# Performance work log

Hardware: AMD Instinct MI355X
Metric: run time of the kernel (lower is better)

Reference implementation:

```python
import jax, jax.numpy as jnp
import numpy as np

EPS = 1e-5
TEMP = 0.07
LARGE_NEG = -1e9


def mi_net(x, W1, g1, b1, W2, b2, Ws, lng, lnb):
    # x: (B, C, T). 1x1 convs == per-position channel projections.
    y = jnp.einsum('bct,oc->bot', x, W1)                      # conv1 (no bias)
    mu = y.mean(axis=(0, 2), keepdims=True)                   # BatchNorm2d, training-mode batch stats
    var = y.var(axis=(0, 2), keepdims=True)
    y = (y - mu) * jax.lax.rsqrt(var + EPS) * g1[None, :, None] + b1[None, :, None]
    y = jax.nn.relu(y)
    y = jnp.einsum('bot,po->bpt', y, W2) + b2[None, :, None]  # conv2 (bias)
    h = y + jnp.einsum('bct,oc->bot', x, Ws)                  # linear shortcut
    mu2 = h.mean(axis=1, keepdims=True)                       # LayerNorm over channel dim
    v2 = h.var(axis=1, keepdims=True)
    return (h - mu2) * jax.lax.rsqrt(v2 + EPS) * lng[None, :, None] + lnb[None, :, None]


def infonce(L, G):
    # L: (N, D, T) locals, G: (N, D) single global per sample (n_multis = 1)
    N, D, T = L.shape
    l_p = jnp.swapaxes(L, 1, 2)                               # (N, T, D)
    l_p = l_p / jnp.linalg.norm(l_p, axis=2, keepdims=True)
    g = G / jnp.linalg.norm(G, axis=1, keepdims=True)         # (N, D)
    u_p = (jnp.einsum('ntd,nd->nt', l_p, g) / TEMP)[:, :, None]   # (N, T, 1), positives scaled by temp
    # negatives: <global_i, local_{j,t}>; NOT divided by temperature (faithful to torch source)
    u_n = jnp.einsum('nd,mtd->nmt', g, l_p)                   # (N, N, T)
    eye = jnp.eye(N, dtype=bool)[:, :, None]
    u_n = jnp.where(eye, LARGE_NEG, u_n).reshape(N, N * T)    # mask self pairs
    logits = jnp.concatenate(
        [u_p, jnp.broadcast_to(u_n[:, None, :], (N, T, N * T))], axis=2)  # (N, T, 1+N*T)
    logp = jax.nn.log_softmax(logits, axis=2)
    return -logp[:, :, 0].mean()


def setup_inputs() -> dict:
    key = jax.random.key(0)
    ks = jax.random.split(key, 10)
    B, CL, CG, T, MI = 32, 1536, 192, 256, 512
    d = {
        'local_feat': jax.random.normal(ks[0], (B, CL, T), jnp.float32),
        'global_feat': jax.random.normal(ks[1], (B, CG), jnp.float32),
        # local_net params
        'lW1': jax.random.normal(ks[2], (MI, CL), jnp.float32) * 0.02,
        'lg1': jnp.ones((MI,), jnp.float32),
        'lb1': jnp.zeros((MI,), jnp.float32),
        'lW2': jax.random.normal(ks[3], (MI, MI), jnp.float32) * 0.02,
        'lb2': jnp.zeros((MI,), jnp.float32),
        'lWs': jax.random.normal(ks[4], (MI, CL), jnp.float32) * 0.02,
        'llng': jnp.ones((MI,), jnp.float32),
        'llnb': jnp.zeros((MI,), jnp.float32),
        # global_net params (global_channels != mi_units -> net exists)
        'gW1': jax.random.normal(ks[5], (MI, CG), jnp.float32) * 0.02,
        'gg1': jnp.ones((MI,), jnp.float32),
        'gb1': jnp.zeros((MI,), jnp.float32),
        'gW2': jax.random.normal(ks[6], (MI, MI), jnp.float32) * 0.02,
        'gb2': jnp.zeros((MI,), jnp.float32),
    }
    # shortcut with near-identity init (n_units >= n_input for global net)
    gWs = jax.random.uniform(ks[7], (MI, CG), jnp.float32, -0.01, 0.01)
    gWs = gWs.at[jnp.arange(CG), jnp.arange(CG)].set(1.0)
    d['gWs'] = gWs
    d['glng'] = jnp.ones((MI,), jnp.float32)
    d['glnb'] = jnp.zeros((MI,), jnp.float32)
    return d


def reference(local_feat, global_feat,
              lW1, lg1, lb1, lW2, lb2, lWs, llng, llnb,
              gW1, gg1, gb1, gW2, gb2, gWs, glng, glnb):
    L = mi_net(local_feat, lW1, lg1, lb1, lW2, lb2, lWs, llng, llnb)      # (B, MI, T)
    G = mi_net(global_feat[:, :, None], gW1, gg1, gb1, gW2, gb2, gWs, glng, glnb)[:, :, 0]  # (B, MI)
    return infonce(L, G)
```

## Files before the change

kernel.cpp:

```cpp
#include <hip/hip_runtime.h>

#define B 32
#define CL 1536
#define CG 192
#define T 256
#define MI 512
#define NPOS 8192
#define EPS 1e-5f
#define TEMP 0.07f

typedef __attribute__((ext_vector_type(8))) __bf16 bf16x8;
typedef __attribute__((ext_vector_type(4))) float f32x4;

__device__ __forceinline__ unsigned short f2bf(float f) {
  union { float f; unsigned u; } v; v.f = f;
  unsigned r = v.u + 0x7FFFu + ((v.u >> 16) & 1u);
  return (unsigned short)(r >> 16);
}
__device__ __forceinline__ float bf2f(unsigned short h) {
  union { unsigned u; float f; } v; v.u = ((unsigned)h) << 16;
  return v.f;
}

__device__ __forceinline__ float wave_sum(float v) {
#pragma unroll
  for (int off = 32; off > 0; off >>= 1) v += __shfl_xor(v, off, 64);
  return v;
}
__device__ __forceinline__ float block_sum(float v, float* rb) {
  v = wave_sum(v);
  __syncthreads();
  if ((threadIdx.x & 63) == 0) rb[threadIdx.x >> 6] = v;
  __syncthreads();
  return rb[0] + rb[1] + rb[2] + rb[3];
}
__device__ __forceinline__ float bs128(float v, float* rb) {
  v = wave_sum(v);
  __syncthreads();
  if ((threadIdx.x & 63) == 0) rb[threadIdx.x >> 6] = v;
  __syncthreads();
  return rb[0] + rb[1];
}

__global__ __launch_bounds__(256) void k_prep(
    const float* __restrict__ x, const float* __restrict__ lW1,
    const float* __restrict__ lWs, const float* __restrict__ lW2,
    const float* __restrict__ gx, const float* __restrict__ gW1,
    unsigned short* __restrict__ xT, unsigned short* __restrict__ Wc,
    unsigned short* __restrict__ W2b, float* __restrict__ y1g,
    float* __restrict__ bsum) {
  __shared__ float xs[64][65];
  const int bi = blockIdx.x, tid = threadIdx.x;
  if (bi < 1792) {
    int idx = (bi * 256 + tid) * 4;
    const float* src; unsigned short* dst;
    if (idx < 786432) { src = lW1 + idx; dst = Wc + idx; }
    else if (idx < 1572864) { src = lWs + (idx - 786432); dst = Wc + idx; }
    else { src = lW2 + (idx - 1572864); dst = W2b + (idx - 1572864); }
    float4 v = *(const float4*)src;
    ushort4 o = {f2bf(v.x), f2bf(v.y), f2bf(v.z), f2bf(v.w)};
    *(ushort4*)dst = o;
  } else if (bi < 4864) {
    int bi2 = bi - 1792;
    int b = bi2 / 96, rem = bi2 - b * 96;
    int c0 = (rem >> 2) * 64, t0 = (rem & 3) * 64;
    const float* xb = x + ((size_t)b * CL + c0) * T + t0;
#pragma unroll
    for (int i = 0; i < 16; i++) {
      int idx = tid + i * 256, c = idx >> 6, t = idx & 63;
      xs[c][t] = xb[(size_t)c * T + t];
    }
    __syncthreads();
    unsigned short* ob = xT + ((size_t)b * T + t0) * CL + c0;
#pragma unroll
    for (int half = 0; half < 2; half++) {
      int s = tid + half * 256;
      int t = s >> 3, kg = s & 7;
      unsigned short v[8];
#pragma unroll
      for (int j = 0; j < 8; j++) v[j] = f2bf(xs[kg * 8 + j][t]);
      uint4 o = {(unsigned)v[0] | ((unsigned)v[1] << 16),
                 (unsigned)v[2] | ((unsigned)v[3] << 16),
                 (unsigned)v[4] | ((unsigned)v[5] << 16),
                 (unsigned)v[6] | ((unsigned)v[7] << 16)};
      *(uint4*)&ob[(size_t)t * CL + kg * 8] = o;
    }
  } else if (bi < 4928) {
    int idx = (bi - 4864) * 256 + tid;
    int b = idx & 31, o = idx >> 5;
    float s = 0.f;
    for (int c = 0; c < CG; c++) s = fmaf(gx[b * CG + c], gW1[o * CG + c], s);
    y1g[o * 32 + b] = s;
  } else {
    float4 z = {0.f, 0.f, 0.f, 0.f};
    ((float4*)bsum)[tid] = z;
  }
}

__global__ __launch_bounds__(128, 2) void k_gemm1(
    const unsigned short* __restrict__ xT, const unsigned short* __restrict__ Wc,
    unsigned short* __restrict__ y1u, unsigned short* __restrict__ ysb,
    float* __restrict__ bsum, float* __restrict__ bsq,
    const float* __restrict__ y1g, const float* __restrict__ gg1,
    const float* __restrict__ gb1, const float* __restrict__ gW2,
    const float* __restrict__ gb2, const float* __restrict__ gx,
    const float* __restrict__ gWsc, float* __restrict__ hg) {
  const int tid = threadIdx.x, bi = blockIdx.x;
  if (bi >= 1024) {
    __shared__ float gsc[512], gsh[512];
#pragma unroll
    for (int jj = 0; jj < 4; jj++) {
      int o = tid + jj * 128;
      float s = 0.f, s2 = 0.f;
      for (int b = 0; b < 32; b++) {
        float v = y1g[o * 32 + b];
        s += v; s2 = fmaf(v, v, s2);
      }
      float mu = s * (1.f / 32.f);
      float var = s2 * (1.f / 32.f) - mu * mu;
      float sc = gg1[o] * rsqrtf(var + EPS);
      gsc[o] = sc;
      gsh[o] = gb1[o] - mu * sc;
    }
    __syncthreads();
    int base = (bi - 1024) * 256;
#pragma unroll
    for (int jj = 0; jj < 2; jj++) {
      int idx = base + jj * 128 + tid;
      int b = idx & 31, p = idx >> 5;
      float s = gb2[p];
      for (int o = 0; o < MI; o++) {
        float v = fmaxf(fmaf(y1g[o * 32 + b], gsc[o], gsh[o]), 0.f);
        s = fmaf(v, gW2[(size_t)p * MI + o], s);
      }
      for (int c = 0; c < CG; c++) s = fmaf(gx[b * CG + c], gWsc[p * CG + c], s);
      hg[p * 32 + b] = s;
    }
    return;
  }
  __shared__ __align__(16) unsigned short As[64 * 64];
  __shared__ __align__(16) unsigned short Bs[128 * 64];
  __shared__ float ps[128], pq[128];
  const int w = tid >> 6, lane = tid & 63;
  const int m0 = (bi & 127) * 64, o0 = (bi >> 7) * 128;
  const int r8 = lane >> 3;
  const int csw = ((lane & 7) ^ r8) * 8;
  const int lm = lane & 15, q = lane >> 4;
  const int sw0 = lm & 7;
  f32x4 acc[4][4];
#pragma unroll
  for (int i = 0; i < 4; i++)
#pragma unroll
    for (int j = 0; j < 4; j++) acc[i][j] = f32x4{0.f, 0.f, 0.f, 0.f};

  const unsigned short* pa = xT + (size_t)(m0 + w * 32 + r8) * CL + csw;
  const unsigned short* pb = Wc + (size_t)(o0 + w * 64 + r8) * CL + csw;
  for (int k0 = 0; k0 < CL; k0 += 64) {
#pragma unroll
    for (int i = 0; i < 4; i++)
      __builtin_amdgcn_global_load_lds(
          (const __attribute__((address_space(1))) void*)(pa + (size_t)i * 8 * CL + k0),
          (__attribute__((address_space(3))) void*)&As[(w * 32 + i * 8) * 64], 16, 0, 0);
#pragma unroll
    for (int i = 0; i < 8; i++)
      __builtin_amdgcn_global_load_lds(
          (const __attribute__((address_space(1))) void*)(pb + (size_t)i * 8 * CL + k0),
          (__attribute__((address_space(3))) void*)&Bs[(w * 64 + i * 8) * 64], 16, 0, 0);
    __syncthreads();
#pragma unroll
    for (int kc = 0; kc < 2; kc++) {
      const int ch = ((kc * 4 + q) ^ sw0) * 8;
      bf16x8 af[4], bfr[4];
#pragma unroll
      for (int mi = 0; mi < 4; mi++)
        af[mi] = *(const bf16x8*)&As[(mi * 16 + lm) * 64 + ch];
#pragma unroll
      for (int ni = 0; ni < 4; ni++)
        bfr[ni] = *(const bf16x8*)&Bs[(w * 64 + ni * 16 + lm) * 64 + ch];
#pragma unroll
      for (int mi = 0; mi < 4; mi++)
#pragma unroll
        for (int ni = 0; ni < 4; ni++)
          acc[mi][ni] = __builtin_amdgcn_mfma_f32_16x16x32_bf16(
              af[mi], bfr[ni], acc[mi][ni], 0, 0, 0);
    }
    __syncthreads();
  }
  const int row0 = m0 + q * 4;
  const bool isY1 = (o0 < 512);
  unsigned short* dst = isY1 ? y1u : ysb;
  const int ob = isY1 ? o0 : o0 - 512;
#pragma unroll
  for (int mi = 0; mi < 4; mi++)
#pragma unroll
    for (int ni = 0; ni < 4; ni++) {
      int oc = ob + w * 64 + ni * 16 + lm;
#pragma unroll
      for (int r = 0; r < 4; r++)
        dst[(size_t)(row0 + mi * 16 + r) * 512 + oc] = f2bf(acc[mi][ni][r]);
    }
  if (isY1) {
#pragma unroll
    for (int ni = 0; ni < 4; ni++) {
      float s = 0.f, s2 = 0.f;
#pragma unroll
      for (int mi = 0; mi < 4; mi++)
#pragma unroll
        for (int r = 0; r < 4; r++) {
          float v = acc[mi][ni][r];
          s += v; s2 = fmaf(v, v, s2);
        }
      s += __shfl_xor(s, 16, 64);  s2 += __shfl_xor(s2, 16, 64);
      s += __shfl_xor(s, 32, 64);  s2 += __shfl_xor(s2, 32, 64);
      if (q == 0) {
        int c = w * 64 + ni * 16 + lm;
        ps[c] = s; pq[c] = s2;
      }
    }
    __syncthreads();
    atomicAdd(&bsum[o0 + tid], ps[tid]);
    atomicAdd(&bsq[o0 + tid], pq[tid]);
  }
}

__global__ __launch_bounds__(128, 2) void k_gemm2(
    const unsigned short* __restrict__ y1u, const unsigned short* __restrict__ W2b,
    const float* __restrict__ bsum, const float* __restrict__ bsq,
    const float* __restrict__ lg1, const float* __restrict__ lb1,
    const float* __restrict__ b2, unsigned short* __restrict__ hb16,
    const float* __restrict__ hg, const float* __restrict__ glng,
    const float* __restrict__ glnb, unsigned short* __restrict__ gnormb) {
  __shared__ __align__(16) unsigned short As[64 * 64];
  __shared__ __align__(16) unsigned short Bs[128 * 64];
  __shared__ float scl[512], shf[512];
  __shared__ float rb[2];
  const int tid = threadIdx.x, bi = blockIdx.x;
  if (bi >= 512) {
    int b = bi - 512;
    float v[4], Lv[4];
    float s = 0.f, s2 = 0.f;
#pragma unroll
    for (int j = 0; j < 4; j++) {
      v[j] = hg[(tid + j * 128) * 32 + b];
      s += v[j]; s2 = fmaf(v[j], v[j], s2);
    }
    s = bs128(s, rb);
    s2 = bs128(s2, rb);
    float mu = s * (1.f / MI);
    float var = s2 * (1.f / MI) - mu * mu;
    float rstd = rsqrtf(var + EPS);
    float n2 = 0.f;
#pragma unroll
    for (int j = 0; j < 4; j++) {
      int p = tid + j * 128;
      Lv[j] = fmaf((v[j] - mu) * rstd, glng[p], glnb[p]);
      n2 = fmaf(Lv[j], Lv[j], n2);
    }
    n2 = bs128(n2, rb);
    float inv = rsqrtf(n2);
#pragma unroll
    for (int j = 0; j < 4; j++)
      gnormb[b * MI + tid + j * 128] = f2bf(Lv[j] * inv);
    return;
  }
  const int w = tid >> 6, lane = tid & 63;
  const int m0 = (bi & 127) * 64, p0 = (bi >> 7) * 128;
  const int r8 = lane >> 3;
  const int csw = ((lane & 7) ^ r8) * 8;
  const int lm = lane & 15, q = lane >> 4;
  const int sw0 = lm & 7;
#pragma unroll
  for (int jj = 0; jj < 4; jj++) {
    int ch = tid + jj * 128;
    float mu = bsum[ch] * (1.f / NPOS);
    float var = bsq[ch] * (1.f / NPOS) - mu * mu;
    float sc = lg1[ch] * rsqrtf(var + EPS);
    scl[ch] = sc;
    shf[ch] = lb1[ch] - mu * sc;
  }
  __syncthreads();
  f32x4 acc[4][4];
#pragma unroll
  for (int i = 0; i < 4; i++)
#pragma unroll
    for (int j = 0; j < 4; j++) acc[i][j] = f32x4{0.f, 0.f, 0.f, 0.f};

  const int cg = tid & 7, rbase = tid >> 3;
  const unsigned short* pb = W2b + (size_t)(p0 + w * 64 + r8) * 512 + csw;
  for (int k0 = 0; k0 < 512; k0 += 64) {
#pragma unroll
    for (int i = 0; i < 8; i++)
      __builtin_amdgcn_global_load_lds(
          (const __attribute__((address_space(1))) void*)(pb + (size_t)i * 8 * 512 + k0),
          (__attribute__((address_space(3))) void*)&Bs[(w * 64 + i * 8) * 64], 16, 0, 0);
    float sreg[8], hreg[8];
#pragma unroll
    for (int j = 0; j < 8; j++) {
      sreg[j] = scl[k0 + cg * 8 + j];
      hreg[j] = shf[k0 + cg * 8 + j];
    }
#pragma unroll
    for (int pass = 0; pass < 4; pass++) {
      int row = rbase + pass * 16;
      uint4 u = *(const uint4*)&y1u[(size_t)(m0 + row) * 512 + k0 + cg * 8];
      unsigned short iv[8] = {
          (unsigned short)(u.x & 0xffff), (unsigned short)(u.x >> 16),
          (unsigned short)(u.y & 0xffff), (unsigned short)(u.y >> 16),
          (unsigned short)(u.z & 0xffff), (unsigned short)(u.z >> 16),
          (unsigned short)(u.w & 0xffff), (unsigned short)(u.w >> 16)};
      unsigned short ov[8];
#pragma unroll
      for (int j = 0; j < 8; j++)
        ov[j] = f2bf(fmaxf(fmaf(bf2f(iv[j]), sreg[j], hreg[j]), 0.f));
      uint4 o = {(unsigned)ov[0] | ((unsigned)ov[1] << 16),
                 (unsigned)ov[2] | ((unsigned)ov[3] << 16),
                 (unsigned)ov[4] | ((unsigned)ov[5] << 16),
                 (unsigned)ov[6] | ((unsigned)ov[7] << 16)};
      *(uint4*)&As[row * 64 + ((cg ^ (row & 7)) * 8)] = o;
    }
    __syncthreads();
#pragma unroll
    for (int kc = 0; kc < 2; kc++) {
      const int ch = ((kc * 4 + q) ^ sw0) * 8;
      bf16x8 af[4], bfr[4];
#pragma unroll
      for (int mi = 0; mi < 4; mi++)
        af[mi] = *(const bf16x8*)&As[(mi * 16 + lm) * 64 + ch];
#pragma unroll
      for (int ni = 0; ni < 4; ni++)
        bfr[ni] = *(const bf16x8*)&Bs[(w * 64 + ni * 16 + lm) * 64 + ch];
#pragma unroll
      for (int mi = 0; mi < 4; mi++)
#pragma unroll
        for (int ni = 0; ni < 4; ni++)
          acc[mi][ni] = __builtin_amdgcn_mfma_f32_16x16x32_bf16(
              af[mi], bfr[ni], acc[mi][ni], 0, 0, 0);
    }
    __syncthreads();
  }
  const int row0 = m0 + q * 4;
#pragma unroll
  for (int ni = 0; ni < 4; ni++) {
    int p = p0 + w * 64 + ni * 16 + lm;
    float bias = b2[p];
#pragma unroll
    for (int mi = 0; mi < 4; mi++)
#pragma unroll
      for (int r = 0; r < 4; r++) {
        size_t off = (size_t)(row0 + mi * 16 + r) * 512 + p;
        hb16[off] = f2bf(acc[mi][ni][r] + bias);
      }
  }
}

__global__ __launch_bounds__(256) void k_tail(
    const unsigned short* __restrict__ hb16, const unsigned short* __restrict__ ysb,
    const float* __restrict__ lng, const float* __restrict__ lnb,
    const unsigned short* __restrict__ gnormb,
    float* __restrict__ up, float* __restrict__ pmax, float* __restrict__ psum) {
  __shared__ __align__(16) unsigned short gs[32 * 512];
  __shared__ __align__(16) unsigned short Ls[32 * 512];
  __shared__ float Ured[4 * 1024];
  const int tid = threadIdx.x;
  const int w = tid >> 6, lane = tid & 63;
  const int r0 = blockIdx.x * 32;
  const int smp = r0 >> 8;
#pragma unroll
  for (int i = 0; i < 8; i++) {
    int e = (tid + i * 256) * 8;
    *(uint4*)&gs[e] = *(const uint4*)&gnormb[e];
  }
  float4 g0 = *(const float4*)&lng[lane * 8];
  float4 g1 = *(const float4*)&lng[lane * 8 + 4];
  float4 bb0 = *(const float4*)&lnb[lane * 8];
  float4 bb1 = *(const float4*)&lnb[lane * 8 + 4];
  float gg[8] = {g0.x, g0.y, g0.z, g0.w, g1.x, g1.y, g1.z, g1.w};
  float bz[8] = {bb0.x, bb0.y, bb0.z, bb0.w, bb1.x, bb1.y, bb1.z, bb1.w};
#pragma unroll
  for (int j = 0; j < 8; j++) {
    int rr = w * 8 + j;
    size_t off = (size_t)(r0 + rr) * 512 + lane * 8;
    uint4 hu = *(const uint4*)&hb16[off];
    uint4 yu = *(const uint4*)&ysb[off];
    unsigned short hv[8] = {
        (unsigned short)(hu.x & 0xffff), (unsigned short)(hu.x >> 16),
        (unsigned short)(hu.y & 0xffff), (unsigned short)(hu.y >> 16),
        (unsigned short)(hu.z & 0xffff), (unsigned short)(hu.z >> 16),
        (unsigned short)(hu.w & 0xffff), (unsigned short)(hu.w >> 16)};
    unsigned short yv[8] = {
        (unsigned short)(yu.x & 0xffff), (unsigned short)(yu.x >> 16),
        (unsigned short)(yu.y & 0xffff), (unsigned short)(yu.y >> 16),
        (unsigned short)(yu.z & 0xffff), (unsigned short)(yu.z >> 16),
        (unsigned short)(yu.w & 0xffff), (unsigned short)(yu.w >> 16)};
    float v[8];
    float s = 0.f, s2 = 0.f;
#pragma unroll
    for (int k = 0; k < 8; k++) {
      v[k] = bf2f(hv[k]) + bf2f(yv[k]);
      s += v[k]; s2 = fmaf(v[k], v[k], s2);
    }
    s = wave_sum(s);
    s2 = wave_sum(s2);
    float mu = s * (1.f / MI);
    float var = s2 * (1.f / MI) - mu * mu;
    float rstd = rsqrtf(var + EPS);
    float L[8], n2 = 0.f;
#pragma unroll
    for (int k = 0; k < 8; k++) {
      L[k] = fmaf((v[k] - mu) * rstd, gg[k], bz[k]);
      n2 = fmaf(L[k], L[k], n2);
    }
    n2 = wave_sum(n2);
    float inv = rsqrtf(n2);
    unsigned short* orow = &Ls[rr * 512 + lane * 8];
    ushort4 o0 = {f2bf(L[0] * inv), f2bf(L[1] * inv), f2bf(L[2] * inv), f2bf(L[3] * inv)};
    ushort4 o1 = {f2bf(L[4] * inv), f2bf(L[5] * inv), f2bf(L[6] * inv), f2bf(L[7] * inv)};
    *(ushort4*)orow = o0;
    *(ushort4*)(orow + 4) = o1;
  }
  __syncthreads();
  const int lm = lane & 15, q = lane >> 4;
  f32x4 acc[2][2];
#pragma unroll
  for (int i = 0; i < 2; i++)
#pragma unroll
    for (int j = 0; j < 2; j++) acc[i][j] = f32x4{0.f, 0.f, 0.f, 0.f};
#pragma unroll
  for (int kk = 0; kk < 4; kk++) {
    int k0 = w * 128 + kk * 32 + q * 8;
    bf16x8 af[2], bfr[2];
#pragma unroll
    for (int mi = 0; mi < 2; mi++)
      af[mi] = *(const bf16x8*)&gs[(mi * 16 + lm) * 512 + k0];
#pragma unroll
    for (int ni = 0; ni < 2; ni++)
      bfr[ni] = *(const bf16x8*)&Ls[(ni * 16 + lm) * 512 + k0];
#pragma unroll
    for (int mi = 0; mi < 2; mi++)
#pragma unroll
      for (int ni = 0; ni < 2; ni++)
        acc[mi][ni] = __builtin_amdgcn_mfma_f32_16x16x32_bf16(
            af[mi], bfr[ni], acc[mi][ni], 0, 0, 0);
  }
#pragma unroll
  for (int mi = 0; mi < 2; mi++)
#pragma unroll
    for (int ni = 0; ni < 2; ni++)
#pragma unroll
      for (int r = 0; r < 4; r++) {
        int m = mi * 16 + q * 4 + r, n = ni * 16 + lm;
        Ured[w * 1024 + m * 32 + n] = acc[mi][ni][r];
      }
  __syncthreads();
  float u[4];
#pragma unroll
  for (int j = 0; j < 4; j++) {
    int idx = tid * 4 + j;
    u[j] = Ured[idx] + Ured[1024 + idx] + Ured[2048 + idx] + Ured[3072 + idx];
  }
  __syncthreads();
#pragma unroll
  for (int j = 0; j < 4; j++) Ured[tid * 4 + j] = u[j];
  int m = (tid * 4) >> 5;
  if (m == smp) {
#pragma unroll
    for (int j = 0; j < 4; j++)
      up[r0 + ((tid * 4 + j) & 31)] = u[j] * (1.f / TEMP);
  }
  __syncthreads();
  if (tid < 32) {
    float mx = -1e30f, s = 0.f;
    if (tid != smp) {
      for (int n = 0; n < 32; n++) mx = fmaxf(mx, Ured[tid * 32 + n]);
      for (int n = 0; n < 32; n++) s += expf(Ured[tid * 32 + n] - mx);
    }
    pmax[tid * 256 + blockIdx.x] = mx;
    psum[tid * 256 + blockIdx.x] = s;
  }
}

__global__ __launch_bounds__(256) void k_loss(
    const float* __restrict__ up, const float* __restrict__ pmax,
    const float* __restrict__ psum, float* __restrict__ out) {
  __shared__ float rb[4];
  __shared__ float red[32][8];
  __shared__ float Ms[32], Ss[32];
  const int tid = threadIdx.x;
  const int n = tid >> 3, j = tid & 7;
  float mx = -1e30f;
  for (int c = j * 32; c < j * 32 + 32; c++) mx = fmaxf(mx, pmax[n * 256 + c]);
  red[n][j] = mx;
  __syncthreads();
  if (j == 0) {
    float M = -1e30f;
#pragma unroll
    for (int k = 0; k < 8; k++) M = fmaxf(M, red[n][k]);
    Ms[n] = M;
  }
  __syncthreads();
  float M = Ms[n];
  float s = 0.f;
  for (int c = j * 32; c < j * 32 + 32; c++)
    s += psum[n * 256 + c] * expf(pmax[n * 256 + c] - M);
  __syncthreads();
  red[n][j] = s;
  __syncthreads();
  if (j == 0) {
    float S = 0.f;
#pragma unroll
    for (int k = 0; k < 8; k++) S += red[n][k];
    Ss[n] = S;
  }
  __syncthreads();
  float acc = 0.f;
  for (int i = tid; i < NPOS; i += 256) {
    int nn = i >> 8;
    float upv = up[i];
    float Mn = Ms[nn], Sn = Ss[nn];
    float mx2 = fmaxf(upv, Mn);
    float lse = mx2 + logf(expf(upv - mx2) + Sn * expf(Mn - mx2));
    acc += lse - upv;
  }
  acc = block_sum(acc, rb);
  if (tid == 0) out[0] = acc * (1.f / NPOS);
}

extern "C" void kernel_launch(void* const* d_in, const int* in_sizes, int n_in,
                              void* d_out, int out_size, void* d_ws, size_t ws_size,
                              hipStream_t stream) {
  (void)in_sizes; (void)n_in; (void)out_size; (void)ws_size;
  const float* x    = (const float*)d_in[0];
  const float* gx   = (const float*)d_in[1];
  const float* lW1  = (const float*)d_in[2];
  const float* lg1  = (const float*)d_in[3];
  const float* lb1  = (const float*)d_in[4];
  const float* lW2  = (const float*)d_in[5];
  const float* lb2  = (const float*)d_in[6];
  const float* lWs  = (const float*)d_in[7];
  const float* llng = (const float*)d_in[8];
  const float* llnb = (const float*)d_in[9];
  const float* gW1  = (const float*)d_in[10];
  const float* gg1  = (const float*)d_in[11];
  const float* gb1  = (const float*)d_in[12];
  const float* gW2  = (const float*)d_in[13];
  const float* gb2  = (const float*)d_in[14];
  const float* gWs  = (const float*)d_in[15];
  const float* glng = (const float*)d_in[16];
  const float* glnb = (const float*)d_in[17];

  char* wsb = (char*)d_ws;
  unsigned short* xT     = (unsigned short*)(wsb);
  unsigned short* Wc     = (unsigned short*)(wsb + 25165824);
  unsigned short* W2b    = (unsigned short*)(wsb + 28311552);
  unsigned short* y1u    = (unsigned short*)(wsb + 28835840);
  unsigned short* ysb    = (unsigned short*)(wsb + 37224448);
  unsigned short* hb16   = (unsigned short*)(wsb + 54001664);
  float* bsum            = (float*)(wsb + 71827456);
  float* bsq             = (float*)(wsb + 71829504);
  float* y1g             = (float*)(wsb + 71831552);
  float* hg              = (float*)(wsb + 71901184);
  unsigned short* gnormb = (unsigned short*)(wsb + 71966720);
  float* up              = (float*)(wsb + 71999488);
  float* pmax            = (float*)(wsb + 72032256);
  float* psum            = (float*)(wsb + 72065024);

  k_prep<<<dim3(4929), 256, 0, stream>>>(x, lW1, lWs, lW2, gx, gW1, xT, Wc, W2b,
                                         y1g, bsum);
  k_gemm1<<<dim3(1088), 128, 0, stream>>>(xT, Wc, y1u, ysb, bsum, bsq,
                                          y1g, gg1, gb1, gW2, gb2, gx, gWs, hg);
  k_gemm2<<<dim3(544), 128, 0, stream>>>(y1u, W2b, bsum, bsq, lg1, lb1, lb2,
                                         hb16, hg, glng, glnb, gnormb);
  k_tail<<<dim3(256), 256, 0, stream>>>(hb16, ysb, llng, llnb, gnormb,
                                        up, pmax, psum);
  k_loss<<<dim3(1), 256, 0, stream>>>(up, pmax, psum, (float*)d_out);
}
```

Before: 233.7 us.

## Fuse conv2 GEMM into tail kernel and shrink gemm1 K-tile

New measurement: 247.7 us. 1.06x slower.

```diff
diff --git a/kernel.cpp b/kernel.cpp
--- a/kernel.cpp
+++ b/kernel.cpp
@@ -33,13 +33,6 @@
   if ((threadIdx.x & 63) == 0) rb[threadIdx.x >> 6] = v;
   __syncthreads();
   return rb[0] + rb[1] + rb[2] + rb[3];
-}
-__device__ __forceinline__ float bs128(float v, float* rb) {
-  v = wave_sum(v);
-  __syncthreads();
-  if ((threadIdx.x & 63) == 0) rb[threadIdx.x >> 6] = v;
-  __syncthreads();
-  return rb[0] + rb[1];
 }
 
 __global__ __launch_bounds__(256) void k_prep(
@@ -97,7 +90,7 @@
   }
 }
 
-__global__ __launch_bounds__(128, 2) void k_gemm1(
+__global__ __launch_bounds__(128, 4) void k_gemm1(
     const unsigned short* __restrict__ xT, const unsigned short* __restrict__ Wc,
     unsigned short* __restrict__ y1u, unsigned short* __restrict__ ysb,
     float* __restrict__ bsum, float* __restrict__ bsq,
@@ -138,52 +131,50 @@
     }
     return;
   }
-  __shared__ __align__(16) unsigned short As[64 * 64];
-  __shared__ __align__(16) unsigned short Bs[128 * 64];
+  __shared__ __align__(16) unsigned short As[64 * 32];
+  __shared__ __align__(16) unsigned short Bs[128 * 32];
   __shared__ float ps[128], pq[128];
   const int w = tid >> 6, lane = tid & 63;
   const int m0 = (bi & 127) * 64, o0 = (bi >> 7) * 128;
-  const int r8 = lane >> 3;
-  const int csw = ((lane & 7) ^ r8) * 8;
+  const int sr = lane >> 2;
+  const int s4d = (sr + (sr >> 2)) & 3;
+  const int csw = (((lane & 3) ^ s4d)) * 8;
   const int lm = lane & 15, q = lane >> 4;
-  const int sw0 = lm & 7;
+  const int s4 = (lm + (lm >> 2)) & 3;
   f32x4 acc[4][4];
 #pragma unroll
   for (int i = 0; i < 4; i++)
 #pragma unroll
     for (int j = 0; j < 4; j++) acc[i][j] = f32x4{0.f, 0.f, 0.f, 0.f};
 
-  const unsigned short* pa = xT + (size_t)(m0 + w * 32 + r8) * CL + csw;
-  const unsigned short* pb = Wc + (size_t)(o0 + w * 64 + r8) * CL + csw;
-  for (int k0 = 0; k0 < CL; k0 += 64) {
+  const unsigned short* pa = xT + (size_t)(m0 + w * 32 + sr) * CL + csw;
+  const unsigned short* pb = Wc + (size_t)(o0 + w * 64 + sr) * CL + csw;
+  for (int k0 = 0; k0 < CL; k0 += 32) {
+    __builtin_amdgcn_global_load_lds(
+        (const __attribute__((address_space(1))) void*)(pa + k0),
+        (__attribute__((address_space(3))) void*)&As[(w * 32) * 32], 16, 0, 0);
+    __builtin_amdgcn_global_load_lds(
+        (const __attribute__((address_space(1))) void*)(pa + 16 * CL + k0),
+        (__attribute__((address_space(3))) void*)&As[(w * 32 + 16) * 32], 16, 0, 0);
 #pragma unroll
     for (int i = 0; i < 4; i++)
       __builtin_amdgcn_global_load_lds(
-          (const __attribute__((address_space(1))) void*)(pa + (size_t)i * 8 * CL + k0),
-          (__attribute__((address_space(3))) void*)&As[(w * 32 + i * 8) * 64], 16, 0, 0);
-#pragma unroll
-    for (int i = 0; i < 8; i++)
-      __builtin_amdgcn_global_load_lds(
-          (const __attribute__((address_space(1))) void*)(pb + (size_t)i * 8 * CL + k0),
-          (__attribute__((address_space(3))) void*)&Bs[(w * 64 + i * 8) * 64], 16, 0, 0);
+          (const __attribute__((address_space(1))) void*)(pb + (size_t)i * 16 * CL + k0),
+          (__attribute__((address_space(3))) void*)&Bs[(w * 64 + i * 16) * 32], 16, 0, 0);
     __syncthreads();
-#pragma unroll
-    for (int kc = 0; kc < 2; kc++) {
-      const int ch = ((kc * 4 + q) ^ sw0) * 8;
-      bf16x8 af[4], bfr[4];
-#pragma unroll
-      for (int mi = 0; mi < 4; mi++)
-        af[mi] = *(const bf16x8*)&As[(mi * 16 + lm) * 64 + ch];
+    bf16x8 af[4], bfr[4];
+#pragma unroll
+    for (int mi = 0; mi < 4; mi++)
+      af[mi] = *(const bf16x8*)&As[(mi * 16 + lm) * 32 + ((q ^ s4) * 8)];
+#pragma unroll
+    for (int ni = 0; ni < 4; ni++)
+      bfr[ni] = *(const bf16x8*)&Bs[(w * 64 + ni * 16 + lm) * 32 + ((q ^ s4) * 8)];
+#pragma unroll
+    for (int mi = 0; mi < 4; mi++)
 #pragma unroll
       for (int ni = 0; ni < 4; ni++)
-        bfr[ni] = *(const bf16x8*)&Bs[(w * 64 + ni * 16 + lm) * 64 + ch];
-#pragma unroll
-      for (int mi = 0; mi < 4; mi++)
-#pragma unroll
-        for (int ni = 0; ni < 4; ni++)
-          acc[mi][ni] = __builtin_amdgcn_mfma_f32_16x16x32_bf16(
-              af[mi], bfr[ni], acc[mi][ni], 0, 0, 0);
-    }
+        acc[mi][ni] = __builtin_amdgcn_mfma_f32_16x16x32_bf16(
+            af[mi], bfr[ni], acc[mi][ni], 0, 0, 0);
     __syncthreads();
   }
   const int row0 = m0 + q * 4;
@@ -223,86 +214,74 @@
   }
 }
 
-__global__ __launch_bounds__(128, 2) void k_gemm2(
-    const unsigned short* __restrict__ y1u, const unsigned short* __restrict__ W2b,
+__global__ __launch_bounds__(256) void k_mid(
+    const float* __restrict__ hg, const float* __restrict__ glng,
+    const float* __restrict__ glnb, unsigned short* __restrict__ gnormb,
     const float* __restrict__ bsum, const float* __restrict__ bsq,
     const float* __restrict__ lg1, const float* __restrict__ lb1,
-    const float* __restrict__ b2, unsigned short* __restrict__ hb16,
-    const float* __restrict__ hg, const float* __restrict__ glng,
-    const float* __restrict__ glnb, unsigned short* __restrict__ gnormb) {
-  __shared__ __align__(16) unsigned short As[64 * 64];
-  __shared__ __align__(16) unsigned short Bs[128 * 64];
-  __shared__ float scl[512], shf[512];
-  __shared__ float rb[2];
-  const int tid = threadIdx.x, bi = blockIdx.x;
-  if (bi >= 512) {
-    int b = bi - 512;
-    float v[4], Lv[4];
-    float s = 0.f, s2 = 0.f;
-#pragma unroll
-    for (int j = 0; j < 4; j++) {
-      v[j] = hg[(tid + j * 128) * 32 + b];
-      s += v[j]; s2 = fmaf(v[j], v[j], s2);
-    }
-    s = bs128(s, rb);
-    s2 = bs128(s2, rb);
+    float* __restrict__ sclT, float* __restrict__ shfT) {
+  __shared__ float rb[4];
+  const int bi = blockIdx.x, tid = threadIdx.x;
+  if (bi < 32) {
+    int b = bi;
+    float v0 = hg[tid * 32 + b];
+    float v1 = hg[(tid + 256) * 32 + b];
+    float s = block_sum(v0 + v1, rb);
+    float s2 = block_sum(fmaf(v0, v0, v1 * v1), rb);
     float mu = s * (1.f / MI);
     float var = s2 * (1.f / MI) - mu * mu;
     float rstd = rsqrtf(var + EPS);
-    float n2 = 0.f;
-#pragma unroll
-    for (int j = 0; j < 4; j++) {
-      int p = tid + j * 128;
-      Lv[j] = fmaf((v[j] - mu) * rstd, glng[p], glnb[p]);
-      n2 = fmaf(Lv[j], Lv[j], n2);
-    }
-    n2 = bs128(n2, rb);
+    float L0 = fmaf((v0 - mu) * rstd, glng[tid], glnb[tid]);
+    float L1 = fmaf((v1 - mu) * rstd, glng[tid + 256], glnb[tid + 256]);
+    float n2 = block_sum(fmaf(L0, L0, L1 * L1), rb);
     float inv = rsqrtf(n2);
-#pragma unroll
-    for (int j = 0; j < 4; j++)
-      gnormb[b * MI + tid + j * 128] = f2bf(Lv[j] * inv);
-    return;
-  }
+    gnormb[b * MI + tid] = f2bf(L0 * inv);
+    gnormb[b * MI + tid + 256] = f2bf(L1 * inv);
+  } else {
+    int o = (bi - 32) * 256 + tid;
+    float mu = bsum[o] * (1.f / NPOS);
+    float var = bsq[o] * (1.f / NPOS) - mu * mu;
+    float sc = lg1[o] * rsqrtf(var + EPS);
+    sclT[o] = sc;
+    shfT[o] = lb1[o] - mu * sc;
+  }
+}
+
+__global__ __launch_bounds__(256, 1) void k_tail(
+    const unsigned short* __restrict__ y1u, const unsigned short* __restrict__ ysb,
+    const unsigned short* __restrict__ W2b, const float* __restrict__ sclT,
+    const float* __restrict__ shfT, const float* __restrict__ b2,
+    const float* __restrict__ lng, const float* __restrict__ lnb,
+    const unsigned short* __restrict__ gnormb,
+    float* __restrict__ up, float* __restrict__ pmax, float* __restrict__ psum) {
+  __shared__ __align__(16) unsigned short vS[32 * 512];
+  __shared__ __align__(16) unsigned short ysS[32 * 512];
+  __shared__ __align__(16) unsigned short Ls[32 * 512];
+  __shared__ float redS[32 * 64];
+  __shared__ float red8[8 * 32];
+  __shared__ float muS[32], rsS[32], invS[32];
+  __shared__ float Ured[4 * 1024];
+  const int tid = threadIdx.x;
   const int w = tid >> 6, lane = tid & 63;
-  const int m0 = (bi & 127) * 64, p0 = (bi >> 7) * 128;
-  const int r8 = lane >> 3;
-  const int csw = ((lane & 7) ^ r8) * 8;
   const int lm = lane & 15, q = lane >> 4;
-  const int sw0 = lm & 7;
-#pragma unroll
-  for (int jj = 0; jj < 4; jj++) {
-    int ch = tid + jj * 128;
-    float mu = bsum[ch] * (1.f / NPOS);
-    float var = bsq[ch] * (1.f / NPOS) - mu * mu;
-    float sc = lg1[ch] * rsqrtf(var + EPS);
-    scl[ch] = sc;
-    shf[ch] = lb1[ch] - mu * sc;
-  }
-  __syncthreads();
-  f32x4 acc[4][4];
-#pragma unroll
-  for (int i = 0; i < 4; i++)
-#pragma unroll
-    for (int j = 0; j < 4; j++) acc[i][j] = f32x4{0.f, 0.f, 0.f, 0.f};
-
-  const int cg = tid & 7, rbase = tid >> 3;
-  const unsigned short* pb = W2b + (size_t)(p0 + w * 64 + r8) * 512 + csw;
-  for (int k0 = 0; k0 < 512; k0 += 64) {
-#pragma unroll
-    for (int i = 0; i < 8; i++)
-      __builtin_amdgcn_global_load_lds(
-          (const __attribute__((address_space(1))) void*)(pb + (size_t)i * 8 * 512 + k0),
-          (__attribute__((address_space(3))) void*)&Bs[(w * 64 + i * 8) * 64], 16, 0, 0);
-    float sreg[8], hreg[8];
-#pragma unroll
-    for (int j = 0; j < 8; j++) {
-      sreg[j] = scl[k0 + cg * 8 + j];
-      hreg[j] = shf[k0 + cg * 8 + j];
-    }
-#pragma unroll
-    for (int pass = 0; pass < 4; pass++) {
-      int row = rbase + pass * 16;
-      uint4 u = *(const uint4*)&y1u[(size_t)(m0 + row) * 512 + k0 + cg * 8];
+  const int r0 = blockIdx.x * 32;
+  const int smp = r0 >> 8;
+
+  {
+    const int row = tid >> 3, seg = tid & 7;
+    const size_t gb = (size_t)(r0 + row) * 512 + seg * 64;
+#pragma unroll
+    for (int c8 = 0; c8 < 8; c8++) {
+      int k8 = seg * 8 + c8;
+      uint4 u = *(const uint4*)&y1u[gb + c8 * 8];
+      uint4 yy = *(const uint4*)&ysb[gb + c8 * 8];
+      int ch = k8 * 8;
+      float4 s0 = *(const float4*)&sclT[ch];
+      float4 s1 = *(const float4*)&sclT[ch + 4];
+      float4 h0 = *(const float4*)&shfT[ch];
+      float4 h1 = *(const float4*)&shfT[ch + 4];
+      float sv[8] = {s0.x, s0.y, s0.z, s0.w, s1.x, s1.y, s1.z, s1.w};
+      float hv[8] = {h0.x, h0.y, h0.z, h0.w, h1.x, h1.y, h1.z, h1.w};
       unsigned short iv[8] = {
           (unsigned short)(u.x & 0xffff), (unsigned short)(u.x >> 16),
           (unsigned short)(u.y & 0xffff), (unsigned short)(u.y >> 16),
@@ -311,137 +290,182 @@
       unsigned short ov[8];
 #pragma unroll
       for (int j = 0; j < 8; j++)
-        ov[j] = f2bf(fmaxf(fmaf(bf2f(iv[j]), sreg[j], hreg[j]), 0.f));
+        ov[j] = f2bf(fmaxf(fmaf(bf2f(iv[j]), sv[j], hv[j]), 0.f));
       uint4 o = {(unsigned)ov[0] | ((unsigned)ov[1] << 16),
                  (unsigned)ov[2] | ((unsigned)ov[3] << 16),
                  (unsigned)ov[4] | ((unsigned)ov[5] << 16),
                  (unsigned)ov[6] | ((unsigned)ov[7] << 16)};
-      *(uint4*)&As[row * 64 + ((cg ^ (row & 7)) * 8)] = o;
-    }
-    __syncthreads();
-#pragma unroll
-    for (int kc = 0; kc < 2; kc++) {
-      const int ch = ((kc * 4 + q) ^ sw0) * 8;
-      bf16x8 af[4], bfr[4];
-#pragma unroll
-      for (int mi = 0; mi < 4; mi++)
-        af[mi] = *(const bf16x8*)&As[(mi * 16 + lm) * 64 + ch];
-#pragma unroll
-      for (int ni = 0; ni < 4; ni++)
-        bfr[ni] = *(const bf16x8*)&Bs[(w * 64 + ni * 16 + lm) * 64 + ch];
-#pragma unroll
-      for (int mi = 0; mi < 4; mi++)
-#pragma unroll
-        for (int ni = 0; ni < 4; ni++)
-          acc[mi][ni] = __builtin_amdgcn_mfma_f32_16x16x32_bf16(
-              af[mi], bfr[ni], acc[mi][ni], 0, 0, 0);
-    }
-    __syncthreads();
-  }
-  const int row0 = m0 + q * 4;
-#pragma unroll
-  for (int ni = 0; ni < 4; ni++) {
-    int p = p0 + w * 64 + ni * 16 + lm;
-    float bias = b2[p];
-#pragma unroll
-    for (int mi = 0; mi < 4; mi++)
-#pragma unroll
-      for (int r = 0; r < 4; r++) {
-        size_t off = (size_t)(row0 + mi * 16 + r) * 512 + p;
-        hb16[off] = f2bf(acc[mi][ni][r] + bias);
-      }
-  }
-}
-
-__global__ __launch_bounds__(256) void k_tail(
-    const unsigned short* __restrict__ hb16, const unsigned short* __restrict__ ysb,
-    const float* __restrict__ lng, const float* __restrict__ lnb,
-    const unsigned short* __restrict__ gnormb,
-    float* __restrict__ up, float* __restrict__ pmax, float* __restrict__ psum) {
-  __shared__ __align__(16) unsigned short gs[32 * 512];
-  __shared__ __align__(16) unsigned short Ls[32 * 512];
-  __shared__ float Ured[4 * 1024];
-  const int tid = threadIdx.x;
-  const int w = tid >> 6, lane = tid & 63;
-  const int r0 = blockIdx.x * 32;
-  const int smp = r0 >> 8;
-#pragma unroll
-  for (int i = 0; i < 8; i++) {
-    int e = (tid + i * 256) * 8;
-    *(uint4*)&gs[e] = *(const uint4*)&gnormb[e];
-  }
-  float4 g0 = *(const float4*)&lng[lane * 8];
-  float4 g1 = *(const float4*)&lng[lane * 8 + 4];
-  float4 bb0 = *(const float4*)&lnb[lane * 8];
-  float4 bb1 = *(const float4*)&lnb[lane * 8 + 4];
-  float gg[8] = {g0.x, g0.y, g0.z, g0.w, g1.x, g1.y, g1.z, g1.w};
-  float bz[8] = {bb0.x, bb0.y, bb0.z, bb0.w, bb1.x, bb1.y, bb1.z, bb1.w};
-#pragma unroll
-  for (int j = 0; j < 8; j++) {
-    int rr = w * 8 + j;
-    size_t off = (size_t)(r0 + rr) * 512 + lane * 8;
-    uint4 hu = *(const uint4*)&hb16[off];
-    uint4 yu = *(const uint4*)&ysb[off];
-    unsigned short hv[8] = {
-        (unsigned short)(hu.x & 0xffff), (unsigned short)(hu.x >> 16),
-        (unsigned short)(hu.y & 0xffff), (unsigned short)(hu.y >> 16),
-        (unsigned short)(hu.z & 0xffff), (unsigned short)(hu.z >> 16),
-        (unsigned short)(hu.w & 0xffff), (unsigned short)(hu.w >> 16)};
-    unsigned short yv[8] = {
-        (unsigned short)(yu.x & 0xffff), (unsigned short)(yu.x >> 16),
-        (unsigned short)(yu.y & 0xffff), (unsigned short)(yu.y >> 16),
-        (unsigned short)(yu.z & 0xffff), (unsigned short)(yu.z >> 16),
-        (unsigned short)(yu.w & 0xffff), (unsigned short)(yu.w >> 16)};
-    float v[8];
-    float s = 0.f, s2 = 0.f;
-#pragma unroll
-    for (int k = 0; k < 8; k++) {
-      v[k] = bf2f(hv[k]) + bf2f(yv[k]);
-      s += v[k]; s2 = fmaf(v[k], v[k], s2);
-    }
-    s = wave_sum(s);
-    s2 = wave_sum(s2);
-    float mu = s * (1.f / MI);
-    float var = s2 * (1.f / MI) - mu * mu;
-    float rstd = rsqrtf(var + EPS);
-    float L[8], n2 = 0.f;
-#pragma unroll
-    for (int k = 0; k < 8; k++) {
-      L[k] = fmaf((v[k] - mu) * rstd, gg[k], bz[k]);
-      n2 = fmaf(L[k], L[k], n2);
-    }
-    n2 = wave_sum(n2);
-    float inv = rsqrtf(n2);
-    unsigned short* orow = &Ls[rr * 512 + lane * 8];
-    ushort4 o0 = {f2bf(L[0] * inv), f2bf(L[1] * inv), f2bf(L[2] * inv), f2bf(L[3] * inv)};
-    ushort4 o1 = {f2bf(L[4] * inv), f2bf(L[5] * inv), f2bf(L[6] * inv), f2bf(L[7] * inv)};
-    *(ushort4*)orow = o0;
-    *(ushort4*)(orow + 4) = o1;
-  }
-  __syncthreads();
-  const int lm = lane & 15, q = lane >> 4;
-  f32x4 acc[2][2];
+      *(uint4*)&vS[row * 512 + ((k8 ^ (row & 7)) * 8)] = o;
+      *(uint4*)&ysS[row * 512 + k8 * 8] = yy;
+    }
+  }
+  __syncthreads();
+
+  f32x4 acc[2][8];
 #pragma unroll
   for (int i = 0; i < 2; i++)
 #pragma unroll
-    for (int j = 0; j < 2; j++) acc[i][j] = f32x4{0.f, 0.f, 0.f, 0.f};
-#pragma unroll
-  for (int kk = 0; kk < 4; kk++) {
-    int k0 = w * 128 + kk * 32 + q * 8;
-    bf16x8 af[2], bfr[2];
+    for (int j = 0; j < 8; j++) acc[i][j] = f32x4{0.f, 0.f, 0.f, 0.f};
+  const unsigned short* pW = W2b + (size_t)(w * 128 + lm) * 512 + q * 8;
+  for (int kc = 0; kc < 16; kc++) {
+    bf16x8 af[2], bfr[8];
 #pragma unroll
     for (int mi = 0; mi < 2; mi++)
-      af[mi] = *(const bf16x8*)&gs[(mi * 16 + lm) * 512 + k0];
-#pragma unroll
-    for (int ni = 0; ni < 2; ni++)
-      bfr[ni] = *(const bf16x8*)&Ls[(ni * 16 + lm) * 512 + k0];
+      af[mi] = *(const bf16x8*)&vS[(mi * 16 + lm) * 512 +
+                                   (((kc * 4 + q) ^ (lm & 7)) * 8)];
+#pragma unroll
+    for (int ni = 0; ni < 8; ni++)
+      bfr[ni] = *(const bf16x8*)(pW + (size_t)ni * 16 * 512 + kc * 32);
 #pragma unroll
     for (int mi = 0; mi < 2; mi++)
 #pragma unroll
-      for (int ni = 0; ni < 2; ni++)
+      for (int ni = 0; ni < 8; ni++)
         acc[mi][ni] = __builtin_amdgcn_mfma_f32_16x16x32_bf16(
             af[mi], bfr[ni], acc[mi][ni], 0, 0, 0);
   }
+  float b2v[8], lngv[8], lnbv[8];
+#pragma unroll
+  for (int ni = 0; ni < 8; ni++) {
+    int p = w * 128 + ni * 16 + lm;
+    b2v[ni] = b2[p];
+    lngv[ni] = lng[p];
+    lnbv[ni] = lnb[p];
+  }
+#pragma unroll
+  for (int mi = 0; mi < 2; mi++)
+#pragma unroll
+    for (int ni = 0; ni < 8; ni++)
+#pragma unroll
+      for (int r = 0; r < 4; r++) {
+        int row = mi * 16 + q * 4 + r;
+        float ys = bf2f(ysS[row * 512 + w * 128 + ni * 16 + lm]);
+        acc[mi][ni][r] += b2v[ni] + ys;
+      }
+#pragma unroll
+  for (int mi = 0; mi < 2; mi++)
+#pragma unroll
+    for (int r = 0; r < 4; r++) {
+      int row = mi * 16 + q * 4 + r;
+      float s = 0.f;
+#pragma unroll
+      for (int ni = 0; ni < 8; ni++) s += acc[mi][ni][r];
+      redS[row * 64 + w * 16 + lm] = s;
+    }
+  __syncthreads();
+  {
+    int rrow = tid & 31, rj = tid >> 5;
+    float p = 0.f;
+#pragma unroll
+    for (int k = 0; k < 8; k++) p += redS[rrow * 64 + rj * 8 + k];
+    red8[rj * 32 + rrow] = p;
+  }
+  __syncthreads();
+  if (tid < 32) {
+    float t = 0.f;
+#pragma unroll
+    for (int j = 0; j < 8; j++) t += red8[j * 32 + tid];
+    muS[tid] = t * (1.f / MI);
+  }
+#pragma unroll
+  for (int mi = 0; mi < 2; mi++)
+#pragma unroll
+    for (int r = 0; r < 4; r++) {
+      int row = mi * 16 + q * 4 + r;
+      float s2 = 0.f;
+#pragma unroll
+      for (int ni = 0; ni < 8; ni++) {
+        float v = acc[mi][ni][r];
+        s2 = fmaf(v, v, s2);
+      }
+      redS[row * 64 + w * 16 + lm] = s2;
+    }
+  __syncthreads();
+  {
+    int rrow = tid & 31, rj = tid >> 5;
+    float p = 0.f;
+#pragma unroll
+    for (int k = 0; k < 8; k++) p += redS[rrow * 64 + rj * 8 + k];
+    red8[rj * 32 + rrow] = p;
+  }
+  __syncthreads();
+  if (tid < 32) {
+    float t = 0.f;
+#pragma unroll
+    for (int j = 0; j < 8; j++) t += red8[j * 32 + tid];
+    float mu = muS[tid];
+    rsS[tid] = rsqrtf(t * (1.f / MI) - mu * mu + EPS);
+  }
+  __syncthreads();
+#pragma unroll
+  for (int mi = 0; mi < 2; mi++)
+#pragma unroll
+    for (int r = 0; r < 4; r++) {
+      int row = mi * 16 + q * 4 + r;
+      float mu = muS[row], rstd = rsS[row];
+      float n2 = 0.f;
+#pragma unroll
+      for (int ni = 0; ni < 8; ni++) {
+        float L = fmaf((acc[mi][ni][r] - mu) * rstd, lngv[ni], lnbv[ni]);
+        n2 = fmaf(L, L, n2);
+      }
+      redS[row * 64 + w * 16 + lm] = n2;
+    }
+  __syncthreads();
+  {
+    int rrow = tid & 31, rj = tid >> 5;
+    float p = 0.f;
+#pragma unroll
+    for (int k = 0; k < 8; k++) p += redS[rrow * 64 + rj * 8 + k];
+    red8[rj * 32 + rrow] = p;
+  }
+  __syncthreads();
+  if (tid < 32) {
+    float t = 0.f;
+#pragma unroll
+    for (int j = 0; j < 8; j++) t += red8[j * 32 + tid];
+    invS[tid] = rsqrtf(t);
+  }
+  __syncthreads();
+#pragma unroll
+  for (int mi = 0; mi < 2; mi++)
+#pragma unroll
+    for (int r = 0; r < 4; r++) {
+      int row = mi * 16 + q * 4 + r;
+      float mu = muS[row], rstd = rsS[row], inv = invS[row];
+#pragma unroll
+      for (int ni = 0; ni < 8; ni++) {
+        int p = w * 128 + ni * 16 + lm;
+        float L = fmaf((acc[mi][ni][r] - mu) * rstd, lngv[ni], lnbv[ni]) * inv;
+        int chunk = p >> 3;
+        Ls[row * 512 + ((chunk ^ (row & 7)) * 8) + (p & 7)] = f2bf(L);
+      }
+    }
+  __syncthreads();
+  f32x4 uacc[2][2];
+#pragma unroll
+  for (int i = 0; i < 2; i++)
+#pragma unroll
+    for (int j = 0; j < 2; j++) uacc[i][j] = f32x4{0.f, 0.f, 0.f, 0.f};
+#pragma unroll
+  for (int kk = 0; kk < 4; kk++) {
+    int k0 = w * 128 + kk * 32;
+    bf16x8 af[2], bfr[2];
+#pragma unroll
+    for (int mi = 0; mi < 2; mi++)
+      af[mi] = *(const bf16x8*)&gnormb[(size_t)(mi * 16 + lm) * 512 + k0 + q * 8];
+#pragma unroll
+    for (int ni = 0; ni < 2; ni++) {
+      int row = ni * 16 + lm;
+      int chunk = (k0 >> 3) + q;
+      bfr[ni] = *(const bf16x8*)&Ls[row * 512 + ((chunk ^ (row & 7)) * 8)];
+    }
+#pragma unroll
+    for (int mi = 0; mi < 2; mi++)
+#pragma unroll
+      for (int ni = 0; ni < 2; ni++)
+        uacc[mi][ni] = __builtin_amdgcn_mfma_f32_16x16x32_bf16(
+            af[mi], bfr[ni], uacc[mi][ni], 0, 0, 0);
+  }
 #pragma unroll
   for (int mi = 0; mi < 2; mi++)
 #pragma unroll
@@ -449,7 +473,7 @@
 #pragma unroll
       for (int r = 0; r < 4; r++) {
         int m = mi * 16 + q * 4 + r, n = ni * 16 + lm;
-        Ured[w * 1024 + m * 32 + n] = acc[mi][ni][r];
+        Ured[w * 1024 + m * 32 + n] = uacc[mi][ni][r];
       }
   __syncthreads();
   float u[4];
@@ -554,23 +578,24 @@
   unsigned short* W2b    = (unsigned short*)(wsb + 28311552);
   unsigned short* y1u    = (unsigned short*)(wsb + 28835840);
   unsigned short* ysb    = (unsigned short*)(wsb + 37224448);
-  unsigned short* hb16   = (unsigned short*)(wsb + 54001664);
-  float* bsum            = (float*)(wsb + 71827456);
-  float* bsq             = (float*)(wsb + 71829504);
-  float* y1g             = (float*)(wsb + 71831552);
-  float* hg              = (float*)(wsb + 71901184);
-  unsigned short* gnormb = (unsigned short*)(wsb + 71966720);
-  float* up              = (float*)(wsb + 71999488);
-  float* pmax            = (float*)(wsb + 72032256);
-  float* psum            = (float*)(wsb + 72065024);
+  float* bsum            = (float*)(wsb + 45613056);
+  float* bsq             = (float*)(wsb + 45615104);
+  float* y1g             = (float*)(wsb + 45617152);
+  float* hg              = (float*)(wsb + 45682688);
+  unsigned short* gnormb = (unsigned short*)(wsb + 45748224);
+  float* up              = (float*)(wsb + 45780992);
+  float* pmax            = (float*)(wsb + 45813760);
+  float* psum            = (float*)(wsb + 45846528);
+  float* sclT            = (float*)(wsb + 45879296);
+  float* shfT            = (float*)(wsb + 45881344);
 
   k_prep<<<dim3(4929), 256, 0, stream>>>(x, lW1, lWs, lW2, gx, gW1, xT, Wc, W2b,
                                          y1g, bsum);
   k_gemm1<<<dim3(1088), 128, 0, stream>>>(xT, Wc, y1u, ysb, bsum, bsq,
                                           y1g, gg1, gb1, gW2, gb2, gx, gWs, hg);
-  k_gemm2<<<dim3(544), 128, 0, stream>>>(y1u, W2b, bsum, bsq, lg1, lb1, lb2,
-                                         hb16, hg, glng, glnb, gnormb);
-  k_tail<<<dim3(256), 256, 0, stream>>>(hb16, ysb, llng, llnb, gnormb,
-                                        up, pmax, psum);
+  k_mid<<<dim3(34), 256, 0, stream>>>(hg, glng, glnb, gnormb, bsum, bsq,
+                                      lg1, lb1, sclT, shfT);
+  k_tail<<<dim3(256), 256, 0, stream>>>(y1u, ysb, W2b, sclT, shfT, lb2,
+                                        llng, llnb, gnormb, up, pmax, psum);
   k_loss<<<dim3(1), 256, 0, stream>>>(up, pmax, psum, (float*)d_out);
 }
```
